# Kernel optimization log

Hardware: AMD Instinct MI355X
Metric: run time of the kernel (lower is better)

The kernel has to match this reference:

```python
import jax, jax.numpy as jnp
import numpy as np

NUM_HEADS = 16
HEAD_DIM = 64  # hidden_dim 1024 / 16 heads
COH_DIM = 8
MOT_RANK = 4


def _linear(x, W, b):
    # torch nn.Linear: y = x @ W.T + b
    return jnp.einsum('...i,oi->...o', x, W) + b


def setup_inputs() -> dict:
    key = jax.random.key(0)
    ks = jax.random.split(key, 17)
    d, c, m = HEAD_DIM, COH_DIM, MOT_RANK
    s = 1.0 / np.sqrt(d)
    sc = 1.0 / np.sqrt(c)
    sm = 1.0 / np.sqrt(m)
    inp = {
        'x': jax.random.normal(ks[0], (4, 2048, 1024), dtype=jnp.float32),
        'Wi': jax.random.uniform(ks[1], (d, d), jnp.float32, -s, s),
        'bi': jax.random.uniform(ks[2], (d,), jnp.float32, -s, s),
        'Wq': jax.random.uniform(ks[3], (d, d), jnp.float32, -s, s),
        'bq': jax.random.uniform(ks[4], (d,), jnp.float32, -s, s),
        'Wk': jax.random.uniform(ks[5], (d, d), jnp.float32, -s, s),
        'bk': jax.random.uniform(ks[6], (d,), jnp.float32, -s, s),
        'Wv': jax.random.uniform(ks[7], (d, d), jnp.float32, -s, s),
        'bv': jax.random.uniform(ks[8], (d,), jnp.float32, -s, s),
        'Wc': jax.random.uniform(ks[9], (c, d), jnp.float32, -s, s),
        'bc': jax.random.uniform(ks[10], (c,), jnp.float32, -s, s),
        'Wci': jax.random.uniform(ks[11], (d, c), jnp.float32, -sc, sc),
        'bci': jax.random.uniform(ks[12], (d,), jnp.float32, -sc, sc),
        'Wm': jax.random.uniform(ks[13], (m, d), jnp.float32, -s, s),
        'bm': jax.random.uniform(ks[14], (m,), jnp.float32, -s, s),
        'Wmi': jax.random.uniform(ks[15], (d, m), jnp.float32, -sm, sm),
        'bmi': jax.random.uniform(ks[16], (d,), jnp.float32, -sm, sm),
    }
    return inp


def reference(x, Wi, bi, Wq, bq, Wk, bk, Wv, bv, Wc, bc, Wci, bci, Wm, bm, Wmi, bmi):
    B, S, D = x.shape
    H, hd = NUM_HEADS, HEAD_DIM
    # split heads: [B, H, S, hd]
    xh = x.reshape(B, S, H, hd).transpose(0, 2, 1, 3)
    # resolution * load_factor = 1.0 scaling (identity here), then input projection
    h = _linear(xh, Wi, bi)
    q = _linear(h, Wq, bq)
    k = _linear(h, Wk, bk)
    v = _linear(h, Wv, bv)
    # scaled dot-product attention per head
    scores = jnp.einsum('bhqd,bhkd->bhqk', q, k) / jnp.sqrt(jnp.float32(hd))
    attn = jax.nn.softmax(scores, axis=-1)
    out = jnp.einsum('bhqk,bhkd->bhqd', attn, v)
    # cohomology round-trip projection
    out = _linear(_linear(out, Wc, bc), Wci, bci)
    # motive round-trip projection
    out = _linear(_linear(out, Wm, bm), Wmi, bmi)
    # merge heads back to [B, S, D]
    return out.transpose(0, 2, 1, 3).reshape(B, S, D)
```

## Files before the change

kernel.cpp:

```cpp
#include <hip/hip_runtime.h>


#define SEQ 2048
#define DM  1024
#define HD  64
#define QS  0.180336880111120429f

typedef short bf16x8 __attribute__((ext_vector_type(8)));
typedef float f32x16 __attribute__((ext_vector_type(16)));

#define MFMA32 __builtin_amdgcn_mfma_f32_32x32x16_bf16

#if defined(__has_builtin)
#if __has_builtin(__builtin_amdgcn_exp2f)
#define EXP2(x) __builtin_amdgcn_exp2f(x)
#endif
#endif
#ifndef EXP2
#define EXP2(x) exp2f(x)
#endif

#define WS_NEED ((size_t)512 + 2ull * 12288)

__device__ __forceinline__ unsigned short f2bf(float f) {
    unsigned int v = __float_as_uint(f);
    unsigned int r = v + 0x7FFFu + ((v >> 16) & 1u);
    return (unsigned short)(r >> 16);
}
__device__ __forceinline__ unsigned int pk2r(float a, float b) {
    return __builtin_amdgcn_perm(__float_as_uint(b) + 0x8000u,
                                 __float_as_uint(a) + 0x8000u, 0x07060302u);
}
__device__ __forceinline__ unsigned int pk2t(float a, float b) {
    return __builtin_amdgcn_perm(__float_as_uint(b), __float_as_uint(a), 0x07060302u);
}
__device__ __forceinline__ unsigned int cvtpk(float a, float b) {
    unsigned int r;
    asm("v_cvt_pk_bf16_f32 %0, %1, %2" : "=v"(r) : "v"(a), "v"(b));
    return r;
}
__device__ __forceinline__ void swap32(unsigned int& a, unsigned int& b) {
    asm("v_permlane32_swap_b32 %0, %1" : "+v"(a), "+v"(b));
}
__device__ __forceinline__ f32x16 z16() {
    f32x16 v;
    #pragma unroll
    for (int i = 0; i < 16; i++) v[i] = 0.f;
    return v;
}

__device__ __forceinline__ void pack2(const f32x16 s, bf16x8& fA, bf16x8& fB) {
    union { bf16x8 v; unsigned int u[4]; } a, b;
    a.u[0] = cvtpk(s[0], s[1]);   a.u[1] = cvtpk(s[2], s[3]);
    a.u[2] = cvtpk(s[4], s[5]);   a.u[3] = cvtpk(s[6], s[7]);
    b.u[0] = cvtpk(s[8], s[9]);   b.u[1] = cvtpk(s[10], s[11]);
    b.u[2] = cvtpk(s[12], s[13]); b.u[3] = cvtpk(s[14], s[15]);
    swap32(a.u[0], a.u[2]); swap32(a.u[1], a.u[3]);
    swap32(b.u[0], b.u[2]); swap32(b.u[1], b.u[3]);
    fA = a.v; fB = b.v;
}

__device__ __forceinline__ void mm16L(const float* __restrict__ wrow,
                                      const float* __restrict__ L, int i0,
                                      float* __restrict__ acc) {
    #pragma unroll
    for (int ii = 0; ii < 16; ii++) acc[ii] = 0.f;
    for (int t = 0; t < 64; t += 4) {
        float4 w4 = *(const float4*)(wrow + t);
        #pragma unroll
        for (int d = 0; d < 4; d++) {
            float wv = (d == 0) ? w4.x : (d == 1) ? w4.y : (d == 2) ? w4.z : w4.w;
            const float* lr = L + (t + d) * 68 + i0;
            float4 a = *(const float4*)lr;
            float4 b = *(const float4*)(lr + 4);
            float4 c = *(const float4*)(lr + 8);
            float4 e = *(const float4*)(lr + 12);
            acc[0] += wv * a.x;  acc[1] += wv * a.y;  acc[2]  += wv * a.z;  acc[3]  += wv * a.w;
            acc[4] += wv * b.x;  acc[5] += wv * b.y;  acc[6]  += wv * b.z;  acc[7]  += wv * b.w;
            acc[8] += wv * c.x;  acc[9] += wv * c.y;  acc[10] += wv * c.z;  acc[11] += wv * c.w;
            acc[12] += wv * e.x; acc[13] += wv * e.y; acc[14] += wv * e.z;  acc[15] += wv * e.w;
        }
    }
}

__global__ __launch_bounds__(256)
void qmt_combine(const float* __restrict__ Wi,  const float* __restrict__ bi,
                 const float* __restrict__ Wq,  const float* __restrict__ bq,
                 const float* __restrict__ Wk,  const float* __restrict__ bk,
                 const float* __restrict__ Wv,  const float* __restrict__ bv,
                 const float* __restrict__ Wc,  const float* __restrict__ bc,
                 const float* __restrict__ Wci, const float* __restrict__ bci,
                 const float* __restrict__ Wm,  const float* __restrict__ bm,
                 const float* __restrict__ Wmi, const float* __restrict__ bmi,
                 float* __restrict__ ws) {
    const int tid = threadIdx.x;
    const int o = tid & 63;
    const int i0 = (tid >> 6) * 16;
    const bool lead = (tid < 64);
    const int role = blockIdx.x;

    __shared__ float Wa_s[64 * 68];
    __shared__ float Wi_s[64 * 68];
    __shared__ float Wvi_s[64 * 68];
    __shared__ float M_s[64 * 68];
    __shared__ float Wc_s[512];
    __shared__ float Wci_s[512];
    __shared__ float Wm_s[256];
    __shared__ float Wmi_s[256];
    __shared__ float bi_s[64], bvi_s[64], c1[64], c2[4];
    __shared__ float U1[32], U2[256];

    unsigned short* wsu = (unsigned short*)(ws + 128);
    const float* Wa = (role == 0) ? Wq : (role == 1) ? Wk : Wv;

    for (int i4 = tid; i4 < 1024; i4 += 256) {
        int r = i4 >> 4, c = (i4 & 15) * 4;
        *(float4*)&Wi_s[r * 68 + c] = *(const float4*)(Wi + i4 * 4);
        *(float4*)&Wa_s[r * 68 + c] = *(const float4*)(Wa + i4 * 4);
    }
    if (role == 2) {
        if (tid < 128) {
            *(float4*)&Wc_s[tid * 4]  = *(const float4*)(Wc + tid * 4);
            *(float4*)&Wci_s[tid * 4] = *(const float4*)(Wci + tid * 4);
        } else if (tid < 192) {
            int t = tid - 128;
            *(float4*)&Wm_s[t * 4]  = *(const float4*)(Wm + t * 4);
            *(float4*)&Wmi_s[t * 4] = *(const float4*)(Wmi + t * 4);
        }
    }
    if (lead) bi_s[o] = bi[o];
    __syncthreads();

    float acc[16];
    if (role == 0) {
        mm16L(Wa_s + o * 68, Wi_s, i0, acc);
        #pragma unroll
        for (int ii = 0; ii < 16; ii++) wsu[o * 64 + i0 + ii] = f2bf(acc[ii] * QS);
        if (lead) {
            float s = bq[o];
            for (int t = 0; t < 64; t++) s += Wa_s[o * 68 + t] * bi_s[t];
            ws[o] = s * QS;
        }
        return;
    }
    if (role == 1) {
        mm16L(Wa_s + o * 68, Wi_s, i0, acc);
        #pragma unroll
        for (int ii = 0; ii < 16; ii++) wsu[4096 + o * 64 + i0 + ii] = f2bf(acc[ii]);
        return;
    }
    mm16L(Wa_s + o * 68, Wi_s, i0, acc);
    #pragma unroll
    for (int ii = 0; ii < 16; ii++) Wvi_s[o * 68 + i0 + ii] = acc[ii];
    if (lead) {
        float s = bv[o];
        for (int t = 0; t < 64; t++) s += Wa_s[o * 68 + t] * bi_s[t];
        bvi_s[o] = s;
    }
    if (tid < 32) {
        int a = tid >> 3, c = tid & 7;
        float s = 0.f;
        for (int t = 0; t < 64; t++) s += Wm_s[a * 64 + t] * Wci_s[t * 8 + c];
        U1[a * 8 + c] = s;
    }
    __syncthreads();
    if (lead) {
        for (int a = 0; a < 4; a++) {
            float s = 0.f;
            for (int cc = 0; cc < 8; cc++) s += U1[a * 8 + cc] * Wc_s[cc * 64 + o];
            U2[a * 64 + o] = s;
        }
        float s = bci[o];
        for (int j = 0; j < 8; j++) s += Wci_s[o * 8 + j] * bc[j];
        c1[o] = s;
    }
    __syncthreads();
    #pragma unroll
    for (int ii = 0; ii < 16; ii++) {
        float s = 0.f;
        for (int a = 0; a < 4; a++) s += Wmi_s[o * 4 + a] * U2[a * 64 + i0 + ii];
        M_s[o * 68 + i0 + ii] = s;
    }
    if (tid < 4) {
        float s = bm[tid];
        for (int i = 0; i < 64; i++) s += Wm_s[tid * 64 + i] * c1[i];
        c2[tid] = s;
    }
    __syncthreads();
    mm16L(M_s + o * 68, Wvi_s, i0, acc);
    #pragma unroll
    for (int ii = 0; ii < 16; ii++) wsu[8192 + o * 64 + i0 + ii] = f2bf(acc[ii]);
    if (lead) {
        float bvv = 0.f;
        for (int t = 0; t < 64; t++) bvv += M_s[o * 68 + t] * bvi_s[t];
        float cvv = bmi[o];
        for (int a = 0; a < 4; a++) cvv += Wmi_s[o * 4 + a] * c2[a];
        ws[64 + o] = cvv + bvv;
    }
}

__global__ __launch_bounds__(256, 3)
void qmt_attn_fb(const float* __restrict__ x, const float* __restrict__ wsf,
                 float* __restrict__ out) {
    __shared__ __align__(16) unsigned short ks_s[64 * 72];
    __shared__ __align__(16) unsigned short vt_s[64 * 72];
    __shared__ float als_l[128];
    __shared__ float ls_l[128];

    const int tid = threadIdx.x;
    const int w = tid >> 6;
    const int lane = tid & 63;
    const int ln = lane & 31;
    const int h = lane >> 5;
    const int b = blockIdx.y >> 4;
    const int hh = blockIdx.y & 15;
    const int qbase = blockIdx.x * 128;

    const unsigned short* wsu = (const unsigned short*)(wsf + 128);

    bf16x8 akf[4], avf[4];
    #pragma unroll
    for (int c = 0; c < 4; c++) {
        int row = (w & 1) * 32 + ln;
        int col = c * 16 + h * 8;
        akf[c] = *(const bf16x8*)(wsu + 4096 + row * 64 + col);
        avf[c] = *(const bf16x8*)(wsu + 8192 + row * 64 + col);
    }
    const float ec0 = wsf[64 + ln];
    const float ec1 = wsf[96 + ln];

    const int krl = (w >> 1) * 32 + ln;
    const int dt32 = (w & 1) * 32;

    float4 xl[8];
    {
        const float* xr = x + ((size_t)(b * SEQ + 0 * 64 + krl) * DM + hh * HD);
        #pragma unroll
        for (int c = 0; c < 4; c++) {
            const float* p = xr + c * 16 + h * 8;
            xl[2 * c]     = *(const float4*)p;
            xl[2 * c + 1] = *(const float4*)(p + 4);
        }
    }

    bf16x8 qf[4];
    {
        bf16x8 xq[4];
        const float* xrow = x + ((size_t)(b * SEQ + qbase + w * 32 + ln) * DM + hh * HD);
        #pragma unroll
        for (int c = 0; c < 4; c++) {
            const float* p = xrow + c * 16 + h * 8;
            float4 f0 = *(const float4*)p;
            float4 f1 = *(const float4*)(p + 4);
            union { bf16x8 v; unsigned int u[4]; } t;
            t.u[0] = pk2t(f0.x, f0.y); t.u[1] = pk2t(f0.z, f0.w);
            t.u[2] = pk2t(f1.x, f1.y); t.u[3] = pk2t(f1.z, f1.w);
            xq[c] = t.v;
        }
        #pragma unroll
        for (int m = 0; m < 2; m++) {
            f32x16 acc;
            #pragma unroll
            for (int g = 0; g < 4; g++) {
                float4 b4 = *(const float4*)&wsf[m * 32 + 8 * g + 4 * h];
                acc[4 * g + 0] = b4.x; acc[4 * g + 1] = b4.y;
                acc[4 * g + 2] = b4.z; acc[4 * g + 3] = b4.w;
            }
            #pragma unroll
            for (int c = 0; c < 4; c++) {
                bf16x8 aq = *(const bf16x8*)(wsu + (m * 32 + ln) * 64 + c * 16 + h * 8);
                acc = MFMA32(aq, xq[c], acc, 0, 0, 0);
            }
            pack2(acc, qf[2 * m], qf[2 * m + 1]);
        }
    }

    f32x16 o0 = z16(), o1 = z16();
    float m_i = -1e30f, l_i = 0.f;

    for (int kt = 0; kt < SEQ / 64; kt++) {
        bf16x8 xf[4];
        #pragma unroll
        for (int c = 0; c < 4; c++) {
            union { bf16x8 v; unsigned int u[4]; } t;
            t.u[0] = pk2t(xl[2 * c].x, xl[2 * c].y);
            t.u[1] = pk2t(xl[2 * c].z, xl[2 * c].w);
            t.u[2] = pk2t(xl[2 * c + 1].x, xl[2 * c + 1].y);
            t.u[3] = pk2t(xl[2 * c + 1].z, xl[2 * c + 1].w);
            xf[c] = t.v;
        }
        f32x16 kacc = z16(), vacc = z16();
        #pragma unroll
        for (int c = 0; c < 4; c++) kacc = MFMA32(akf[c], xf[c], kacc, 0, 0, 0);
        #pragma unroll
        for (int c = 0; c < 4; c++) vacc = MFMA32(xf[c], avf[c], vacc, 0, 0, 0);
        #pragma unroll
        for (int g = 0; g < 4; g++) {
            uint2 pk_, pv_;
            pk_.x = pk2r(kacc[4 * g + 0], kacc[4 * g + 1]);
            pk_.y = pk2r(kacc[4 * g + 2], kacc[4 * g + 3]);
            *(uint2*)&ks_s[krl * 72 + dt32 + 8 * g + 4 * h] = pk_;
            pv_.x = pk2r(vacc[4 * g + 0], vacc[4 * g + 1]);
            pv_.y = pk2r(vacc[4 * g + 2], vacc[4 * g + 3]);
            *(uint2*)&vt_s[(dt32 + ln) * 72 + (w >> 1) * 32 + 8 * g + 4 * h] = pv_;
        }
        if (kt + 1 < SEQ / 64) {
            const float* xr = x + ((size_t)(b * SEQ + (kt + 1) * 64 + krl) * DM + hh * HD);
            #pragma unroll
            for (int c = 0; c < 4; c++) {
                const float* p = xr + c * 16 + h * 8;
                xl[2 * c]     = *(const float4*)p;
                xl[2 * c + 1] = *(const float4*)(p + 4);
            }
        }
        __syncthreads();

        f32x16 st0 = z16(), st1 = z16();
        #pragma unroll
        for (int c = 0; c < 4; c++) {
            bf16x8 k0 = *(const bf16x8*)&ks_s[ln * 72 + c * 16 + h * 8];
            bf16x8 k1 = *(const bf16x8*)&ks_s[(32 + ln) * 72 + c * 16 + h * 8];
            st0 = MFMA32(k0, qf[c], st0, 0, 0, 0);
            st1 = MFMA32(k1, qf[c], st1, 0, 0, 0);
        }
        float tm[8];
        #pragma unroll
        for (int i = 0; i < 8; i++)
            tm[i] = fmaxf(fmaxf(st0[i], st0[i + 8]), fmaxf(st1[i], st1[i + 8]));
        #pragma unroll
        for (int i = 0; i < 4; i++) tm[i] = fmaxf(tm[i], tm[i + 4]);
        float mx = fmaxf(fmaxf(tm[0], tm[1]), fmaxf(tm[2], tm[3]));
        mx = fmaxf(mx, __shfl_xor(mx, 32));
        const float mn = fmaxf(m_i, mx);
        const float al = EXP2(m_i - mn);
        float ss = 0.f;
        #pragma unroll
        for (int i = 0; i < 16; i++) { st0[i] = EXP2(st0[i] - mn); ss += st0[i]; }
        #pragma unroll
        for (int i = 0; i < 16; i++) { st1[i] = EXP2(st1[i] - mn); ss += st1[i]; }
        ss += __shfl_xor(ss, 32);
        l_i = l_i * al + ss;
        m_i = mn;
        if (lane < 32) als_l[w * 32 + lane] = al;

        bf16x8 pf[4];
        pack2(st0, pf[0], pf[1]);
        pack2(st1, pf[2], pf[3]);

        #pragma unroll
        for (int g = 0; g < 4; g++) {
            float4 a4 = *(const float4*)&als_l[w * 32 + 8 * g + 4 * h];
            o0[4 * g + 0] *= a4.x; o0[4 * g + 1] *= a4.y;
            o0[4 * g + 2] *= a4.z; o0[4 * g + 3] *= a4.w;
            o1[4 * g + 0] *= a4.x; o1[4 * g + 1] *= a4.y;
            o1[4 * g + 2] *= a4.z; o1[4 * g + 3] *= a4.w;
        }
        #pragma unroll
        for (int c = 0; c < 4; c++) {
            bf16x8 v0 = *(const bf16x8*)&vt_s[ln * 72 + c * 16 + h * 8];
            bf16x8 v1 = *(const bf16x8*)&vt_s[(32 + ln) * 72 + c * 16 + h * 8];
            o0 = MFMA32(pf[c], v0, o0, 0, 0, 0);
            o1 = MFMA32(pf[c], v1, o1, 0, 0, 0);
        }
        __syncthreads();
    }

    if (lane < 32) ls_l[w * 32 + lane] = l_i;
    #pragma unroll
    for (int g = 0; g < 4; g++) {
        float4 l4 = *(const float4*)&ls_l[w * 32 + 8 * g + 4 * h];
        float4 iv = make_float4(1.f / l4.x, 1.f / l4.y, 1.f / l4.z, 1.f / l4.w);
        #pragma unroll
        for (int i = 0; i < 4; i++) {
            float ivv = (i == 0) ? iv.x : (i == 1) ? iv.y : (i == 2) ? iv.z : iv.w;
            int q = qbase + w * 32 + 8 * g + 4 * h + i;
            float* orow = out + ((size_t)(b * SEQ + q) * DM + hh * HD);
            orow[ln] = o0[4 * g + i] * ivv + ec0;
            orow[32 + ln] = o1[4 * g + i] * ivv + ec1;
        }
    }
}

extern "C" void kernel_launch(void* const* d_in, const int* in_sizes, int n_in,
                              void* d_out, int out_size, void* d_ws, size_t ws_size,
                              hipStream_t stream) {
    const float* x = (const float*)d_in[0];
    float* wsf = (float*)d_ws;
    (void)ws_size;

    qmt_combine<<<3, 256, 0, stream>>>(
        (const float*)d_in[1],  (const float*)d_in[2],
        (const float*)d_in[3],  (const float*)d_in[4],
        (const float*)d_in[5],  (const float*)d_in[6],
        (const float*)d_in[7],  (const float*)d_in[8],
        (const float*)d_in[9],  (const float*)d_in[10],
        (const float*)d_in[11], (const float*)d_in[12],
        (const float*)d_in[13], (const float*)d_in[14],
        (const float*)d_in[15], (const float*)d_in[16],
        wsf);

    dim3 grid(SEQ / 128, 64);
    qmt_attn_fb<<<grid, 256, 0, stream>>>(x, wsf, (float*)d_out);
}
```

Before: 281.9 us.

## Double-buffer K/V tiles in shared memory and raise occupancy bound

Result: slower. 403.2 us (+43.0%).

```diff
diff --git a/kernel.cpp b/kernel.cpp
--- a/kernel.cpp
+++ b/kernel.cpp
@@ -199,11 +199,11 @@
     }
 }
 
-__global__ __launch_bounds__(256, 3)
+__global__ __launch_bounds__(256, 4)
 void qmt_attn_fb(const float* __restrict__ x, const float* __restrict__ wsf,
                  float* __restrict__ out) {
-    __shared__ __align__(16) unsigned short ks_s[64 * 72];
-    __shared__ __align__(16) unsigned short vt_s[64 * 72];
+    __shared__ __align__(16) unsigned short ks_s[2][64 * 72];
+    __shared__ __align__(16) unsigned short vt_s[2][64 * 72];
     __shared__ float als_l[128];
     __shared__ float ls_l[128];
 
@@ -278,7 +278,7 @@
     f32x16 o0 = z16(), o1 = z16();
     float m_i = -1e30f, l_i = 0.f;
 
-    for (int kt = 0; kt < SEQ / 64; kt++) {
+    {
         bf16x8 xf[4];
         #pragma unroll
         for (int c = 0; c < 4; c++) {
@@ -299,27 +299,68 @@
             uint2 pk_, pv_;
             pk_.x = pk2r(kacc[4 * g + 0], kacc[4 * g + 1]);
             pk_.y = pk2r(kacc[4 * g + 2], kacc[4 * g + 3]);
-            *(uint2*)&ks_s[krl * 72 + dt32 + 8 * g + 4 * h] = pk_;
+            *(uint2*)&ks_s[0][krl * 72 + dt32 + 8 * g + 4 * h] = pk_;
             pv_.x = pk2r(vacc[4 * g + 0], vacc[4 * g + 1]);
             pv_.y = pk2r(vacc[4 * g + 2], vacc[4 * g + 3]);
-            *(uint2*)&vt_s[(dt32 + ln) * 72 + (w >> 1) * 32 + 8 * g + 4 * h] = pv_;
-        }
+            *(uint2*)&vt_s[0][(dt32 + ln) * 72 + (w >> 1) * 32 + 8 * g + 4 * h] = pv_;
+        }
+        const float* xr = x + ((size_t)(b * SEQ + 1 * 64 + krl) * DM + hh * HD);
+        #pragma unroll
+        for (int c = 0; c < 4; c++) {
+            const float* p = xr + c * 16 + h * 8;
+            xl[2 * c]     = *(const float4*)p;
+            xl[2 * c + 1] = *(const float4*)(p + 4);
+        }
+    }
+    __syncthreads();
+
+    for (int kt = 0; kt < SEQ / 64; kt++) {
+        const int cur = kt & 1;
         if (kt + 1 < SEQ / 64) {
-            const float* xr = x + ((size_t)(b * SEQ + (kt + 1) * 64 + krl) * DM + hh * HD);
+            bf16x8 xf[4];
             #pragma unroll
             for (int c = 0; c < 4; c++) {
-                const float* p = xr + c * 16 + h * 8;
-                xl[2 * c]     = *(const float4*)p;
-                xl[2 * c + 1] = *(const float4*)(p + 4);
+                union { bf16x8 v; unsigned int u[4]; } t;
+                t.u[0] = pk2t(xl[2 * c].x, xl[2 * c].y);
+                t.u[1] = pk2t(xl[2 * c].z, xl[2 * c].w);
+                t.u[2] = pk2t(xl[2 * c + 1].x, xl[2 * c + 1].y);
+                t.u[3] = pk2t(xl[2 * c + 1].z, xl[2 * c + 1].w);
+                xf[c] = t.v;
             }
-        }
-        __syncthreads();
+            f32x16 kacc = z16(), vacc = z16();
+            #pragma unroll
+            for (int c = 0; c < 4; c++) kacc = MFMA32(akf[c], xf[c], kacc, 0, 0, 0);
+            #pragma unroll
+            for (int c = 0; c < 4; c++) vacc = MFMA32(xf[c], avf[c], vacc, 0, 0, 0);
+            #pragma unroll
+            for (int g = 0; g < 4; g++) {
+                uint2 pk_, pv_;
+                pk_.x = pk2r(kacc[4 * g + 0], kacc[4 * g + 1]);
+                pk_.y = pk2r(kacc[4 * g + 2], kacc[4 * g + 3]);
+                *(uint2*)&ks_s[cur ^ 1][krl * 72 + dt32 + 8 * g + 4 * h] = pk_;
+                pv_.x = pk2r(vacc[4 * g + 0], vacc[4 * g + 1]);
+                pv_.y = pk2r(vacc[4 * g + 2], vacc[4 * g + 3]);
+                *(uint2*)&vt_s[cur ^ 1][(dt32 + ln) * 72 + (w >> 1) * 32 + 8 * g + 4 * h] = pv_;
+            }
+            if (kt + 2 < SEQ / 64) {
+                const float* xr = x + ((size_t)(b * SEQ + (kt + 2) * 64 + krl) * DM + hh * HD);
+                #pragma unroll
+                for (int c = 0; c < 4; c++) {
+                    const float* p = xr + c * 16 + h * 8;
+                    xl[2 * c]     = *(const float4*)p;
+                    xl[2 * c + 1] = *(const float4*)(p + 4);
+                }
+            }
+        }
+
+        const unsigned short* ks = ks_s[cur];
+        const unsigned short* vt = vt_s[cur];
 
         f32x16 st0 = z16(), st1 = z16();
         #pragma unroll
         for (int c = 0; c < 4; c++) {
-            bf16x8 k0 = *(const bf16x8*)&ks_s[ln * 72 + c * 16 + h * 8];
-            bf16x8 k1 = *(const bf16x8*)&ks_s[(32 + ln) * 72 + c * 16 + h * 8];
+            bf16x8 k0 = *(const bf16x8*)&ks[ln * 72 + c * 16 + h * 8];
+            bf16x8 k1 = *(const bf16x8*)&ks[(32 + ln) * 72 + c * 16 + h * 8];
             st0 = MFMA32(k0, qf[c], st0, 0, 0, 0);
             st1 = MFMA32(k1, qf[c], st1, 0, 0, 0);
         }
@@ -357,8 +398,8 @@
         }
         #pragma unroll
         for (int c = 0; c < 4; c++) {
-            bf16x8 v0 = *(const bf16x8*)&vt_s[ln * 72 + c * 16 + h * 8];
-            bf16x8 v1 = *(const bf16x8*)&vt_s[(32 + ln) * 72 + c * 16 + h * 8];
+            bf16x8 v0 = *(const bf16x8*)&vt[ln * 72 + c * 16 + h * 8];
+            bf16x8 v1 = *(const bf16x8*)&vt[(32 + ln) * 72 + c * 16 + h * 8];
             o0 = MFMA32(pf[c], v0, o0, 0, 0, 0);
             o1 = MFMA32(pf[c], v1, o1, 0, 0, 0);
         }
```
